# Kernel tuning notes

Measured on AMD Instinct MI355X. Metric: run time of the kernel, lower is better.

Reference implementation:

```python
import jax, jax.numpy as jnp
import numpy as np

N = 100000
E = 1600000
F_IN = 128
HID = 128
EMB = 128
P_DROP = 0.1
NEG_SLOPE = 0.01  # torch leaky_relu default


def setup_inputs() -> dict:
    key = jax.random.key(0)
    ks = jax.random.split(key, 8)
    x = jax.random.normal(ks[0], (N, F_IN), dtype=jnp.float32)
    edge_index = jax.random.randint(ks[1], (2, E), 0, N, dtype=jnp.int64)
    s = 1.0 / np.sqrt(F_IN)
    W1 = jax.random.uniform(ks[2], (F_IN, HID), jnp.float32, -s, s)
    b1 = jnp.zeros((HID,), jnp.float32)
    s2 = 1.0 / np.sqrt(HID)
    W2 = jax.random.uniform(ks[3], (HID, EMB), jnp.float32, -s2, s2)
    b2 = jnp.zeros((EMB,), jnp.float32)
    s3 = 1.0 / np.sqrt(EMB)
    Wl = jax.random.uniform(ks[4], (EMB, 1), jnp.float32, -s3, s3)
    bl = jnp.zeros((1,), jnp.float32)
    return {"x": x, "edge_index": edge_index, "W1": W1, "b1": b1,
            "W2": W2, "b2": b2, "Wl": Wl, "bl": bl}


def _gcn_conv(x, W, b, src, dst, dinv_sqrt):
    # PyG GCNConv: h = x W; out = D^-1/2 (A + I) D^-1/2 h + b
    h = x @ W                                   # [N, F]
    norm = dinv_sqrt[src] * dinv_sqrt[dst]      # [E]
    agg = jax.ops.segment_sum(h[src] * norm[:, None], dst, num_segments=N)
    agg = agg + h * (dinv_sqrt * dinv_sqrt)[:, None]  # self-loop term
    return agg + b


def _dropout(x, key, p):
    keep = jax.random.bernoulli(key, 1.0 - p, x.shape)
    return jnp.where(keep, x / (1.0 - p), 0.0)


def reference(x, edge_index, W1, b1, W2, b2, Wl, bl):
    src, dst = edge_index[0], edge_index[1]
    # degree with self-loops (edge weight 1)
    deg = jax.ops.segment_sum(jnp.ones((E,), x.dtype), dst, num_segments=N) + 1.0
    dinv_sqrt = jax.lax.rsqrt(deg)

    dk1, dk2 = jax.random.split(jax.random.key(42))
    h = _gcn_conv(x, W1, b1, src, dst, dinv_sqrt)
    h = jax.nn.leaky_relu(h, NEG_SLOPE)
    h = _dropout(h, dk1, P_DROP)
    h = _gcn_conv(h, W2, b2, src, dst, dinv_sqrt)
    h = jax.nn.leaky_relu(h, NEG_SLOPE)
    h = _dropout(h, dk2, P_DROP)
    out = h @ Wl + bl                           # [N, 1]
    return out.reshape(-1)                      # [N]
```

## Files before the change

kernel.cpp:

```cpp
#include <hip/hip_runtime.h>
#include <hip/hip_fp16.h>
#include <stdint.h>

#define NN 100000
#define EE 1600000
#define FD 128
#define ELLCAP 64
#define NB 782
#define CHUNK 8192
#define NBLK 196
#define SMEM_BYTES 45120

typedef _Float16 half8 __attribute__((ext_vector_type(8)));
typedef float    floatx4 __attribute__((ext_vector_type(4)));

struct TF2 { uint32_t x0, x1; };

__host__ __device__ constexpr uint32_t rotl32c(uint32_t x, int d) {
  return (x << d) | (x >> (32 - d));
}

__host__ __device__ constexpr TF2 threefry2x32(uint32_t k0, uint32_t k1,
                                               uint32_t c0, uint32_t c1) {
  const uint32_t ks2 = k0 ^ k1 ^ 0x1BD11BDAu;
  uint32_t x0 = c0 + k0;
  uint32_t x1 = c1 + k1;
  const int r0[4] = {13, 15, 26, 6};
  const int r1[4] = {17, 29, 16, 24};
  for (int i = 0; i < 4; i++) { x0 += x1; x1 = rotl32c(x1, r0[i]); x1 ^= x0; }
  x0 += k1;  x1 += ks2 + 1u;
  for (int i = 0; i < 4; i++) { x0 += x1; x1 = rotl32c(x1, r1[i]); x1 ^= x0; }
  x0 += ks2; x1 += k0 + 2u;
  for (int i = 0; i < 4; i++) { x0 += x1; x1 = rotl32c(x1, r0[i]); x1 ^= x0; }
  x0 += k0;  x1 += k1 + 3u;
  for (int i = 0; i < 4; i++) { x0 += x1; x1 = rotl32c(x1, r1[i]); x1 ^= x0; }
  x0 += k1;  x1 += ks2 + 4u;
  for (int i = 0; i < 4; i++) { x0 += x1; x1 = rotl32c(x1, r0[i]); x1 ^= x0; }
  x0 += ks2; x1 += k0 + 5u;
  return TF2{x0, x1};
}

constexpr TF2 DK1 = threefry2x32(0u, 42u, 0u, 0u);
constexpr TF2 DK2 = threefry2x32(0u, 42u, 0u, 1u);

__device__ __forceinline__ float drop_scale(uint32_t k0, uint32_t k1, uint32_t m) {
  TF2 r = threefry2x32(k0, k1, 0u, m);
  const uint32_t bits = r.x0 ^ r.x1;
  float u = __uint_as_float((bits >> 9) | 0x3f800000u) - 1.0f;
  return (u < 0.9f) ? (1.0f / 0.9f) : 0.0f;
}

__device__ __forceinline__ void scatter_body(char* smem, int bid,
                                             const int* __restrict__ src,
                                             const int* __restrict__ dst,
                                             int* __restrict__ ebuf,
                                             unsigned* __restrict__ tcnt) {
  unsigned* sHist = (unsigned*)smem;
  unsigned* sScan = sHist + 1024;
  unsigned* sCur  = sScan + 1024;
  unsigned* sPart = sCur + 784;
  int*      sPay  = (int*)(sPart + 256);
  const int tid  = threadIdx.x;
  const int base = bid * CHUNK;

  for (int i = tid; i < 1024; i += 256) sHist[i] = 0u;
  __syncthreads();

#pragma unroll
  for (int j = 0; j < CHUNK / 256; ++j) {
    const int e = base + j * 256 + tid;
    if (e < EE) atomicAdd(&sHist[dst[e] >> 7], 1u);
  }
  __syncthreads();

  {
    const unsigned s0 = sHist[4 * tid + 0];
    const unsigned s1 = sHist[4 * tid + 1];
    const unsigned s2 = sHist[4 * tid + 2];
    const unsigned s3 = sHist[4 * tid + 3];
    sPart[tid] = s0 + s1 + s2 + s3;
    __syncthreads();
    for (int off = 1; off < 256; off <<= 1) {
      unsigned v = 0u;
      if (tid >= off) v = sPart[tid - off];
      __syncthreads();
      if (tid >= off) sPart[tid] += v;
      __syncthreads();
    }
    const unsigned excl = (tid == 0) ? 0u : sPart[tid - 1];
    sScan[4 * tid + 0] = excl;
    sScan[4 * tid + 1] = excl + s0;
    sScan[4 * tid + 2] = excl + s0 + s1;
    sScan[4 * tid + 3] = excl + s0 + s1 + s2;
  }
  for (int i = tid; i < NB; i += 256) sCur[i] = 0u;
  __syncthreads();

#pragma unroll
  for (int j = 0; j < CHUNK / 256; ++j) {
    const int e = base + j * 256 + tid;
    if (e < EE) {
      const int s = src[e];
      const int d = dst[e];
      const int b = d >> 7;
      const unsigned p = sScan[b] + atomicAdd(&sCur[b], 1u);
      sPay[p] = ((d & 127) << 17) | s;
    }
  }
  __syncthreads();

  {
    int4* g = (int4*)(ebuf + (size_t)bid * CHUNK);
    const int4* l = (const int4*)sPay;
#pragma unroll
    for (int i = tid; i < CHUNK / 4; i += 256) g[i] = l[i];
    for (int b = tid; b < NB; b += 256)
      tcnt[bid * 1024 + b] = (sScan[b] << 14) | sHist[b];
  }
}

template <typename IN>
__device__ __forceinline__ void gemm_body(char* smem, int bid,
                                          const IN* __restrict__ X,
                                          const float* __restrict__ W,
                                          __half* __restrict__ H) {
  _Float16 (*sWT)[136] = (_Float16(*)[136])smem;
  const int tid  = threadIdx.x;
  const int wave = tid >> 6;
  const int lane = tid & 63;
  const int quad = lane >> 4;
  const int m    = lane & 15;
  const int row0 = bid * 128;

  {
    const int n = tid & 127, g = tid >> 7;
#pragma unroll 4
    for (int j = 0; j < 32; ++j) {
      const int k = (g * 32 + j) * 2;
      union { _Float16 h[2]; uint32_t u; } p;
      p.h[0] = (_Float16)W[k * 128 + n];
      p.h[1] = (_Float16)W[(k + 1) * 128 + n];
      *(uint32_t*)&sWT[n][k] = p.u;
    }
  }
  __syncthreads();

  floatx4 acc[2][8];
#pragma unroll
  for (int rt = 0; rt < 2; ++rt)
#pragma unroll
    for (int ct = 0; ct < 8; ++ct) acc[rt][ct] = (floatx4){0.f, 0.f, 0.f, 0.f};

#pragma unroll
  for (int kk = 0; kk < 4; ++kk) {
    const int kb = kk * 32 + quad * 8;
    half8 a[2];
#pragma unroll
    for (int rt = 0; rt < 2; ++rt) {
      int gr = row0 + wave * 32 + rt * 16 + m;
      if (gr >= NN) gr = NN - 1;
      if constexpr (sizeof(IN) == 4) {
        const float4 lo = *(const float4*)(X + (size_t)gr * 128 + kb);
        const float4 hi = *(const float4*)(X + (size_t)gr * 128 + kb + 4);
        a[rt][0] = (_Float16)lo.x; a[rt][1] = (_Float16)lo.y;
        a[rt][2] = (_Float16)lo.z; a[rt][3] = (_Float16)lo.w;
        a[rt][4] = (_Float16)hi.x; a[rt][5] = (_Float16)hi.y;
        a[rt][6] = (_Float16)hi.z; a[rt][7] = (_Float16)hi.w;
      } else {
        a[rt] = *(const half8*)(X + (size_t)gr * 128 + kb);
      }
    }
#pragma unroll
    for (int ct = 0; ct < 8; ++ct) {
      const half8 b = *(const half8*)&sWT[ct * 16 + m][kb];
      acc[0][ct] = __builtin_amdgcn_mfma_f32_16x16x32_f16(a[0], b, acc[0][ct], 0, 0, 0);
      acc[1][ct] = __builtin_amdgcn_mfma_f32_16x16x32_f16(a[1], b, acc[1][ct], 0, 0, 0);
    }
  }

  __syncthreads();
#pragma unroll
  for (int rt = 0; rt < 2; ++rt)
#pragma unroll
    for (int reg = 0; reg < 4; ++reg) {
      const int row = wave * 32 + rt * 16 + quad * 4 + reg;
#pragma unroll
      for (int ct = 0; ct < 8; ++ct)
        sWT[row][ct * 16 + m] = (_Float16)acc[rt][ct][reg];
    }
  __syncthreads();
#pragma unroll
  for (int c = 0; c < 8; ++c) {
    const int chunk = tid + c * 256;
    const int row = chunk >> 4;
    const int seg = chunk & 15;
    const int gr = row0 + row;
    if (gr < NN)
      *(half8*)(H + (size_t)gr * 128 + seg * 8) =
          *(const half8*)&sWT[row][seg * 8];
  }
}

__global__ __launch_bounds__(256) void k_g1s(const float* __restrict__ X,
                                             const float* __restrict__ W,
                                             __half* __restrict__ H,
                                             const int* __restrict__ src,
                                             const int* __restrict__ dst,
                                             int* __restrict__ ebuf,
                                             unsigned* __restrict__ tcnt) {
  __shared__ __align__(16) char smem[SMEM_BYTES];
  if (blockIdx.x < NBLK) {
    scatter_body(smem, blockIdx.x, src, dst, ebuf, tcnt);
  } else {
    gemm_body<float>(smem, blockIdx.x - NBLK, X, W, H);
  }
}

__global__ __launch_bounds__(256) void k_gemm2(const __half* __restrict__ X,
                                               const float* __restrict__ W,
                                               __half* __restrict__ H) {
  __shared__ __align__(16) char smem[34816];
  gemm_body<__half>(smem, blockIdx.x, X, W, H);
}

__global__ __launch_bounds__(256) void k_build(const unsigned* __restrict__ tcnt,
                                               const int* __restrict__ ebuf,
                                               int* __restrict__ ell,
                                               unsigned* __restrict__ deg,
                                               float* __restrict__ dinv) {
  __shared__ int      sEll[128 * ELLCAP];
  __shared__ unsigned sFill[128];
  const int b   = blockIdx.x;
  const int tid = threadIdx.x;
  if (tid < 128) sFill[tid] = 0u;
  __syncthreads();

  for (int x = tid; x < NBLK; x += 256) {
    const unsigned t   = tcnt[x * 1024 + b];
    const unsigned off = t >> 14;
    const unsigned c   = t & 16383u;
    const int* p = ebuf + (size_t)x * CHUNK + off;
    for (unsigned i = 0; i < c; ++i) {
      const int pay = p[i];
      const int dl = (pay >> 17) & 127;
      const unsigned sl = atomicAdd(&sFill[dl], 1u);
      if (sl < ELLCAP) sEll[dl * ELLCAP + sl] = pay & 0x1FFFF;
    }
  }
  __syncthreads();

  const int node0 = b * 128;
  const int limRows = (NN - node0) < 128 ? (NN - node0) : 128;
  int4* g = (int4*)(ell + (size_t)node0 * ELLCAP);
  const int4* l = (const int4*)sEll;
  const int limV = limRows * (ELLCAP / 4);
  for (int i = tid; i < limV; i += 256) g[i] = l[i];
  if (tid < 128 && node0 + tid < NN) {
    const unsigned d = sFill[tid];
    deg[node0 + tid] = d;
    dinv[node0 + tid] = 1.0f / sqrtf((float)d + 1.0f);
  }
}

template <int LAYER>
__global__ __launch_bounds__(256) void k_agg(const __half* __restrict__ H,
                                             const int* __restrict__ ell,
                                             const unsigned* __restrict__ degc,
                                             const float* __restrict__ dinv,
                                             const float* __restrict__ bias,
                                             const float* __restrict__ Wl,
                                             const float* __restrict__ bl,
                                             void* __restrict__ outv) {
  const int tid  = threadIdx.x;
  const int lane = tid & 63;
  const int n    = blockIdx.x * 4 + (tid >> 6);

  const float di = dinv[n];
  const __half2* __restrict__ H2 = (const __half2*)H;
  const char*    __restrict__ Hb = (const char*)H;

  unsigned cnt = degc[n];
  if (cnt > ELLCAP) cnt = ELLCAP;
  const int m = (int)cnt;
  int srcl = 0; float dl = 0.0f;
  if (lane < m) { srcl = ell[(size_t)n * ELLCAP + lane]; dl = dinv[srcl] * di; }
  const int wb = __float_as_int(dl);

  const uint32_t k0 = (LAYER == 1) ? DK1.x0 : DK2.x0;
  const uint32_t k1 = (LAYER == 1) ? DK1.x1 : DK2.x1;
  const uint32_t mb = (uint32_t)n * 128u + (uint32_t)lane * 2u;
  const float ds0 = drop_scale(k0, k1, mb + 0u);
  const float ds1 = drop_scale(k0, k1, mb + 1u);

  const float2 hv = __half22float2(H2[(size_t)n * 64 + lane]);
  const float sw = di * di;

  const int q    = lane >> 4;
  const int coff = (lane & 15) * 16;

  float acc[8];
#pragma unroll
  for (int r = 0; r < 8; ++r) acc[r] = 0.0f;

  for (int i = 0; i < m; i += 16) {
    int4 g[4];
#pragma unroll
    for (int k = 0; k < 4; ++k) {
      const int idx = i + 4 * k + q;
      const unsigned s_ = (unsigned)__shfl(srcl, idx, 64);
      g[k] = *(const int4*)(Hb + (s_ * 256u + (unsigned)coff));
    }
    __builtin_amdgcn_sched_barrier(0);
#pragma unroll
    for (int k = 0; k < 4; ++k) {
      const int idx = i + 4 * k + q;
      const float w_ = __int_as_float(__shfl(wb, idx, 64));
      const __half2* hp = (const __half2*)&g[k];
#pragma unroll
      for (int t = 0; t < 4; ++t) {
        const float2 f = __half22float2(hp[t]);
        acc[2 * t]     = fmaf(w_, f.x, acc[2 * t]);
        acc[2 * t + 1] = fmaf(w_, f.y, acc[2 * t + 1]);
      }
    }
  }

#pragma unroll
  for (int r = 0; r < 8; ++r) {
    acc[r] += __shfl_xor(acc[r], 16, 64);
    acc[r] += __shfl_xor(acc[r], 32, 64);
  }
  const int srcLane = lane >> 2;
  float b_[8];
#pragma unroll
  for (int r = 0; r < 8; ++r) b_[r] = __shfl(acc[r], srcLane, 64);
  const int t2 = lane & 3;
  float a0 = (t2 == 0) ? b_[0] : (t2 == 1) ? b_[2] : (t2 == 2) ? b_[4] : b_[6];
  float a1 = (t2 == 0) ? b_[1] : (t2 == 1) ? b_[3] : (t2 == 2) ? b_[5] : b_[7];
  a0 = fmaf(hv.x, sw, a0);
  a1 = fmaf(hv.y, sw, a1);

  const float2 b = ((const float2*)bias)[lane];
  float v0 = a0 + b.x, v1 = a1 + b.y;
  v0 = v0 >= 0.f ? v0 : 0.01f * v0;
  v1 = v1 >= 0.f ? v1 : 0.01f * v1;

  v0 *= ds0;
  v1 *= ds1;

  if constexpr (LAYER == 1) {
    __half2* out = (__half2*)outv;
    out[(size_t)n * 64 + lane] = __floats2half2_rn(v0, v1);
  } else {
    float* out = (float*)outv;
    const float2 wl = ((const float2*)Wl)[lane];
    float p = v0 * wl.x + v1 * wl.y;
#pragma unroll
    for (int d = 32; d > 0; d >>= 1) p += __shfl_down(p, d, 64);
    if (lane == 0) out[n] = p + bl[0];
  }
}

extern "C" void kernel_launch(void* const* d_in, const int* in_sizes, int n_in,
                              void* d_out, int out_size, void* d_ws, size_t ws_size,
                              hipStream_t stream) {
  const float* x  = (const float*)d_in[0];
  const int*   ei = (const int*)d_in[1];
  const float* W1 = (const float*)d_in[2];
  const float* b1 = (const float*)d_in[3];
  const float* W2 = (const float*)d_in[4];
  const float* b2 = (const float*)d_in[5];
  const float* Wl = (const float*)d_in[6];
  const float* bl = (const float*)d_in[7];
  float* out = (float*)d_out;

  unsigned* deg  = (unsigned*)d_ws;
  float*    dinv = (float*)(deg + NN);
  int*      ell  = (int*)(dinv + NN);
  __half*   bufA = (__half*)(ell + (size_t)NN * ELLCAP);
  __half*   bufB = bufA + (size_t)NN * FD;
  int*      ebuf = (int*)bufB;
  unsigned* tcnt = (unsigned*)(ebuf + (size_t)NBLK * CHUNK);

  const int* srcI = ei;
  const int* dstI = ei + EE;

  const int gemmGrid = (NN + 127) / 128;
  k_g1s<<<NBLK + gemmGrid, 256, 0, stream>>>(x, W1, bufA, srcI, dstI,
                                             ebuf, tcnt);
  k_build<<<NB, 256, 0, stream>>>(tcnt, ebuf, ell, deg, dinv);
  k_agg<1><<<NN / 4, 256, 0, stream>>>(bufA, ell, deg, dinv,
                                       b1, nullptr, nullptr, bufB);
  k_gemm2<<<gemmGrid, 256, 0, stream>>>(bufB, W2, bufA);
  k_agg<2><<<NN / 4, 256, 0, stream>>>(bufA, ell, deg, dinv,
                                       b2, Wl, bl, out);
}
```

Baseline: 283.1 us.

## Fuse layer-1 aggregation with layer-2 GEMM in one kernel

Replaces the separate layer-1 aggregation kernel and the second GEMM kernel with a single kernel. Each block aggregates 128 rows (bias, leaky ReLU, dropout), stages them in shared memory as fp16, then multiplies by W2 with MFMA and writes H2 directly. This removes the intermediate activation write/read round trip and one launch. In exchange it uses 68 KB of LDS and only 782 blocks of 4 waves each doing 32 rows of gathers sequentially, which may reduce latency hiding for the irregular gathers, and W2 is transposed into LDS per block.

```diff
diff --git a/kernel.cpp b/kernel.cpp
--- a/kernel.cpp
+++ b/kernel.cpp
@@ -216,13 +216,6 @@
   }
 }
 
-__global__ __launch_bounds__(256) void k_gemm2(const __half* __restrict__ X,
-                                               const float* __restrict__ W,
-                                               __half* __restrict__ H) {
-  __shared__ __align__(16) char smem[34816];
-  gemm_body<__half>(smem, blockIdx.x, X, W, H);
-}
-
 __global__ __launch_bounds__(256) void k_build(const unsigned* __restrict__ tcnt,
                                                const int* __restrict__ ebuf,
                                                int* __restrict__ ell,
@@ -259,6 +252,129 @@
     const unsigned d = sFill[tid];
     deg[node0 + tid] = d;
     dinv[node0 + tid] = 1.0f / sqrtf((float)d + 1.0f);
+  }
+}
+
+__global__ __launch_bounds__(256) void k_ag12(const __half* __restrict__ H,
+                                              const int* __restrict__ ell,
+                                              const unsigned* __restrict__ degc,
+                                              const float* __restrict__ dinv,
+                                              const float* __restrict__ bias,
+                                              const float* __restrict__ W,
+                                              __half* __restrict__ Hout) {
+  __shared__ __align__(16) char smem[69632];
+  _Float16 (*sWT)[136] = (_Float16(*)[136])smem;
+  _Float16 (*sY)[136]  = (_Float16(*)[136])(smem + 34816);
+  const int tid  = threadIdx.x;
+  const int wave = tid >> 6;
+  const int lane = tid & 63;
+  const int quad = lane >> 4;
+  const int ml   = lane & 15;
+  const int row0 = blockIdx.x * 128;
+
+  {
+    const int n = tid & 127, g = tid >> 7;
+#pragma unroll 4
+    for (int j = 0; j < 32; ++j) {
+      const int k = (g * 32 + j) * 2;
+      union { _Float16 h[2]; uint32_t u; } p;
+      p.h[0] = (_Float16)W[k * 128 + n];
+      p.h[1] = (_Float16)W[(k + 1) * 128 + n];
+      *(uint32_t*)&sWT[n][k] = p.u;
+    }
+  }
+
+  const __half2* __restrict__ H2 = (const __half2*)H;
+  const uint32_t ul = (uint32_t)lane;
+  for (int j = 0; j < 32; ++j) {
+    const int r = wave * 32 + j;
+    const int n = row0 + r;
+    float v0 = 0.0f, v1 = 0.0f;
+    if (n < NN) {
+      const float di = dinv[n];
+      unsigned cnt = degc[n];
+      if (cnt > ELLCAP) cnt = ELLCAP;
+      const int m = (int)cnt;
+      int srcl = 0; float dl = 0.0f;
+      if (lane < m) { srcl = ell[(size_t)n * ELLCAP + lane]; dl = dinv[srcl] * di; }
+      const int wb = __float_as_int(dl);
+
+      const uint32_t mb = (uint32_t)n * 128u + (uint32_t)lane * 2u;
+      const float ds0 = drop_scale(DK1.x0, DK1.x1, mb + 0u);
+      const float ds1 = drop_scale(DK1.x0, DK1.x1, mb + 1u);
+
+      const float2 hv = __half22float2(H2[(size_t)n * 64 + lane]);
+      const float sw = di * di;
+      float a0 = hv.x * sw, a1 = hv.y * sw;
+
+      for (int i = 0; i < m; i += 8) {
+        __half2 g[8];
+#pragma unroll
+        for (int k = 0; k < 8; ++k) {
+          const uint32_t s_ = (uint32_t)__builtin_amdgcn_readlane(srcl, i + k);
+          g[k] = H2[s_ * 64u + ul];
+        }
+        __builtin_amdgcn_sched_barrier(0);
+#pragma unroll
+        for (int k = 0; k < 8; ++k) {
+          const float w_ = __int_as_float(__builtin_amdgcn_readlane(wb, i + k));
+          a0 = fmaf(w_, __low2float(g[k]), a0);
+          a1 = fmaf(w_, __high2float(g[k]), a1);
+        }
+      }
+
+      const float2 b = ((const float2*)bias)[lane];
+      v0 = a0 + b.x; v1 = a1 + b.y;
+      v0 = v0 >= 0.f ? v0 : 0.01f * v0;
+      v1 = v1 >= 0.f ? v1 : 0.01f * v1;
+      v0 *= ds0; v1 *= ds1;
+    }
+    sY[r][2 * lane]     = (_Float16)v0;
+    sY[r][2 * lane + 1] = (_Float16)v1;
+  }
+  __syncthreads();
+
+  floatx4 acc[2][8];
+#pragma unroll
+  for (int rt = 0; rt < 2; ++rt)
+#pragma unroll
+    for (int ct = 0; ct < 8; ++ct) acc[rt][ct] = (floatx4){0.f, 0.f, 0.f, 0.f};
+
+#pragma unroll
+  for (int kk = 0; kk < 4; ++kk) {
+    const int kb = kk * 32 + quad * 8;
+    half8 a[2];
+#pragma unroll
+    for (int rt = 0; rt < 2; ++rt)
+      a[rt] = *(const half8*)&sY[wave * 32 + rt * 16 + ml][kb];
+#pragma unroll
+    for (int ct = 0; ct < 8; ++ct) {
+      const half8 b = *(const half8*)&sWT[ct * 16 + ml][kb];
+      acc[0][ct] = __builtin_amdgcn_mfma_f32_16x16x32_f16(a[0], b, acc[0][ct], 0, 0, 0);
+      acc[1][ct] = __builtin_amdgcn_mfma_f32_16x16x32_f16(a[1], b, acc[1][ct], 0, 0, 0);
+    }
+  }
+
+  __syncthreads();
+#pragma unroll
+  for (int rt = 0; rt < 2; ++rt)
+#pragma unroll
+    for (int reg = 0; reg < 4; ++reg) {
+      const int row = wave * 32 + rt * 16 + quad * 4 + reg;
+#pragma unroll
+      for (int ct = 0; ct < 8; ++ct)
+        sWT[row][ct * 16 + ml] = (_Float16)acc[rt][ct][reg];
+    }
+  __syncthreads();
+#pragma unroll
+  for (int c = 0; c < 8; ++c) {
+    const int chunk = tid + c * 256;
+    const int row = chunk >> 4;
+    const int seg = chunk & 15;
+    const int gr = row0 + row;
+    if (gr < NN)
+      *(half8*)(Hout + (size_t)gr * 128 + seg * 8) =
+          *(const half8*)&sWT[row][seg * 8];
   }
 }
 
@@ -389,9 +505,8 @@
   k_g1s<<<NBLK + gemmGrid, 256, 0, stream>>>(x, W1, bufA, srcI, dstI,
                                              ebuf, tcnt);
   k_build<<<NB, 256, 0, stream>>>(tcnt, ebuf, ell, deg, dinv);
-  k_agg<1><<<NN / 4, 256, 0, stream>>>(bufA, ell, deg, dinv,
-                                       b1, nullptr, nullptr, bufB);
-  k_gemm2<<<gemmGrid, 256, 0, stream>>>(bufB, W2, bufA);
-  k_agg<2><<<NN / 4, 256, 0, stream>>>(bufA, ell, deg, dinv,
+  k_ag12<<<gemmGrid, 256, 0, stream>>>(bufA, ell, deg, dinv,
+                                       b1, W2, bufB);
+  k_agg<2><<<NN / 4, 256, 0, stream>>>(bufB, ell, deg, dinv,
                                        b2, Wl, bl, out);
 }
```

Measured after the change: 398.7 us. 1.41x slower.
